# Kernel optimization log

Hardware: AMD Instinct MI355X
Metric: run time of the kernel (lower is better)

The kernel has to match this reference:

```python
import jax, jax.numpy as jnp
import numpy as np

EPS = 1e-5
HEADS = 8


def _bn(x, p):
    # p: [4, C] rows = (gamma, beta, running_mean, running_var); channel axis = 1 (eval-mode BN)
    shape = (1, p.shape[1]) + (1,) * (x.ndim - 2)
    g = p[0].reshape(shape); b = p[1].reshape(shape)
    m = p[2].reshape(shape); v = p[3].reshape(shape)
    return (x - m) * (g / jnp.sqrt(v + EPS)) + b


def _conv1x1(x, w):
    # x: [N, Cin, H, W], w: [Cout, Cin]
    return jnp.einsum('oc,nchw->nohw', w, x)


def _axial(x, kqv_w, kqv_bn, logits_bn, rel_enc, ks, height_dim):
    # x: [B, C, H, W]
    if height_dim:
        x = jnp.transpose(x, (0, 3, 1, 2))  # [B, W, C, H] -> attend over H (=ks)
    else:
        x = jnp.transpose(x, (0, 2, 1, 3))  # [B, H, C, W] -> attend over W (=ks)
    b, w, d, h = x.shape
    dh = d // HEADS
    xf = x.reshape(b * w, d, h)
    kqv = jnp.einsum('oc,ncl->nol', kqv_w, xf)          # conv1d k=1, [n, 2d, h]
    kqv = _bn(kqv, kqv_bn)
    kqv = kqv.reshape(b * w, HEADS, dh * 2, h)
    k = kqv[:, :, : dh // 2]                            # [n, H, dh/2, h]
    q = kqv[:, :, dh // 2: dh]                          # [n, H, dh/2, h]
    v = kqv[:, :, dh:]                                  # [n, H, dh,   h]
    # relative position encodings
    idx = jnp.arange(ks)[None, :] - jnp.arange(ks)[:, None] + ks - 1  # [ks, ks]
    rel = rel_enc[:, idx.reshape(-1)].reshape(dh * 2, ks, ks)
    q_enc = rel[: dh // 2]
    k_enc = rel[dh // 2: dh]
    v_enc = rel[dh:]
    qk = jnp.einsum('nhdx,nhdy->nhxy', q, k)
    qr = jnp.einsum('nhdx,dxy->nhxy', q, q_enc)
    kr = jnp.einsum('nhdx,dxy->nhyx', k, k_enc)         # einsum + transpose(2,3)
    logits = jnp.concatenate([qk, qr, kr], axis=1)       # [n, 3*H, h, h]
    logits = _bn(logits, logits_bn)
    logits = logits.reshape(b * w, 3, HEADS, h, h).sum(axis=1)
    weights = jax.nn.softmax(logits, axis=3)             # [n, H, h, h]
    attn = jnp.einsum('nhxy,nhdy->nhdx', weights, v)
    attn_enc = jnp.einsum('nhxy,dxy->nhdx', weights, v_enc)
    # cat along last dim + reshape + sum(dim=-2) in torch == elementwise sum here
    out = (attn + attn_enc).reshape(b, w, d, h)
    if height_dim:
        out = jnp.transpose(out, (0, 2, 3, 1))  # [B, C, H, W]
    else:
        out = jnp.transpose(out, (0, 2, 1, 3))  # [B, C, H, W]
    return out


def setup_inputs() -> dict:
    key = jax.random.key(0)
    ks = jax.random.split(key, 13)
    def rn(k, shape, s=0.05):
        return jax.random.normal(k, shape, jnp.float32) * s
    def rp(k, shape):
        return jax.random.uniform(k, shape, jnp.float32, minval=0.1, maxval=1.0)
    return {
        'x': jax.random.normal(ks[0], (1, 64, 256, 128), jnp.float32),
        'conv1_w': rn(ks[1], (64, 64)),
        'bn1': rp(ks[2], (4, 64)),
        'kqv_w_h': rn(ks[3], (128, 64)),
        'kqv_bn_h': rp(ks[4], (4, 128)),
        'logits_bn_h': rp(ks[5], (4, 24)),
        'rel_enc_h': rn(ks[6], (16, 511)),
        'kqv_w_w': rn(ks[7], (128, 64)),
        'kqv_bn_w': rp(ks[8], (4, 128)),
        'logits_bn_w': rp(ks[9], (4, 24)),
        'rel_enc_w': rn(ks[10], (16, 255)),
        'conv3_w': rn(ks[11], (64, 64)),
        'bn3': rp(ks[12], (4, 64)),
    }


def reference(x, conv1_w, bn1, kqv_w_h, kqv_bn_h, logits_bn_h, rel_enc_h,
              kqv_w_w, kqv_bn_w, logits_bn_w, rel_enc_w, conv3_w, bn3):
    out = jax.nn.relu(_bn(_conv1x1(x, conv1_w), bn1))
    out = _axial(out, kqv_w_h, kqv_bn_h, logits_bn_h, rel_enc_h, 256, True)
    out = _axial(out, kqv_w_w, kqv_bn_w, logits_bn_w, rel_enc_w, 128, False)
    out = jax.nn.relu(out)
    out = _bn(_conv1x1(out, conv3_w), bn3)
    return jax.nn.relu(out + x)
```

## Files before the change

### kernel.cpp

```cpp
#include <hip/hip_runtime.h>
#include <stdint.h>

#define EPSF 1e-5f
#define LOG2E 1.4426950408889634f

typedef float f32x2 __attribute__((ext_vector_type(2)));
typedef float f32x4 __attribute__((ext_vector_type(4)));

__device__ __forceinline__ float bflo(uint32_t u){ union{uint32_t u;float f;}c; c.u=u<<16; return c.f; }
__device__ __forceinline__ float bfhi(uint32_t u){ union{uint32_t u;float f;}c; c.u=u&0xffff0000u; return c.f; }
__device__ __forceinline__ float bfhiraw(uint32_t u){ union{uint32_t u;float f;}c; c.u=u; return c.f; }
__device__ __forceinline__ uint32_t f2bf(float f){ union{float f;uint32_t u;}c; c.f=f; uint32_t u=c.u; return (u + 0x7fffu + ((u>>16)&1u)) >> 16; }
__device__ __forceinline__ uint32_t pk2(float a, float b){ return f2bf(a) | (f2bf(b)<<16); }

__global__ void k_relpack(const float* __restrict__ relH, const float* __restrict__ relW,
                          uint4* __restrict__ rqkH, uint4* __restrict__ rveH,
                          uint4* __restrict__ rqkW, uint4* __restrict__ rveW) {
  int NJ = blockIdx.x ? 255 : 511;
  const float* rel = blockIdx.x ? relW : relH;
  uint4* rqk = blockIdx.x ? rqkW : rqkH;
  uint4* rve = blockIdx.x ? rveW : rveH;
  int j = threadIdx.x;
  if (j >= NJ) return;
  const float* q = rel;
  const float* k = rel + 4*NJ;
  const float* v = rel + 8*NJ;
  int jr = NJ-1-j;
  uint4 a;
  a.x = pk2(q[0*NJ+j], q[1*NJ+j]);
  a.y = pk2(q[2*NJ+j], q[3*NJ+j]);
  a.z = pk2(k[0*NJ+jr], k[1*NJ+jr]);
  a.w = pk2(k[2*NJ+jr], k[3*NJ+jr]);
  rqk[j] = a;
  uint4 b;
  b.x = pk2(v[0*NJ+j], v[1*NJ+j]);
  b.y = pk2(v[2*NJ+j], v[3*NJ+j]);
  b.z = pk2(v[4*NJ+j], v[5*NJ+j]);
  b.w = pk2(v[6*NJ+j], v[7*NJ+j]);
  rve[j] = b;
}

__global__ __launch_bounds__(256)
void k_conv1(const float* __restrict__ in, const float* __restrict__ w,
             const float* __restrict__ bn, float* __restrict__ out) {
  __shared__ float L[64*65];
  int tid = threadIdx.x;
  int p0 = blockIdx.x * 64;
  int lane = tid & 63;
  int wvs = __builtin_amdgcn_readfirstlane(tid >> 6);
  #pragma unroll
  for (int rr = 0; rr < 16; ++rr) {
    int c = wvs*16 + rr;
    L[lane*65 + c] = in[(size_t)c*32768 + p0 + lane];
  }
  __syncthreads();
  f32x2 xv2[32];
  #pragma unroll
  for (int c2 = 0; c2 < 32; ++c2) {
    xv2[c2].x = L[lane*65 + 2*c2];
    xv2[c2].y = L[lane*65 + 2*c2 + 1];
  }
  float val[16];
  #pragma unroll
  for (int r = 0; r < 16; ++r) {
    int o = wvs*16 + r;
    const f32x2* wr = (const f32x2*)(w + o*64);
    f32x2 a2 = {0.f, 0.f};
    #pragma unroll
    for (int c2 = 0; c2 < 32; ++c2) a2 = wr[c2]*xv2[c2] + a2;
    float acc = a2.x + a2.y;
    float s = bn[o] * rsqrtf(bn[192+o] + EPSF);
    val[r] = fmaxf(fmaf(acc, s, fmaf(-bn[128+o], s, bn[64+o])), 0.f);
  }
  __syncthreads();
  #pragma unroll
  for (int r = 0; r < 16; ++r) L[lane*65 + wvs*16 + r] = val[r];
  __syncthreads();
  float4* dst = (float4*)(out + (size_t)p0*64);
  #pragma unroll
  for (int k = 0; k < 4; ++k) {
    int f4 = tid + k*256;
    int f = f4*4; int p = f >> 6, o = f & 63;
    float4 v;
    v.x = L[p*65+o]; v.y = L[p*65+o+1]; v.z = L[p*65+o+2]; v.w = L[p*65+o+3];
    dst[f4] = v;
  }
}

template<int LEN, int RS, int CS>
__global__ __launch_bounds__(512)
void k_kqv(const float* __restrict__ in, const float* __restrict__ w,
           const float* __restrict__ bn, uint4* __restrict__ kvV,
           uint2* __restrict__ kvK, float* __restrict__ qb) {
  __shared__ float L[64*65];
  int tid = threadIdx.x;
  int n = blockIdx.x;
  int y0 = blockIdx.y * 64;
  #pragma unroll
  for (int rr = 0; rr < 8; ++rr) {
    int idx = tid + rr*512;
    int yy = idx >> 6, c = idx & 63;
    L[yy*65 + c] = in[((size_t)(y0+yy)*RS + (size_t)n*CS)*64 + c];
  }
  __syncthreads();
  int hd = __builtin_amdgcn_readfirstlane(tid >> 6);
  int yy = tid & 63;
  f32x2 xv2[32];
  #pragma unroll
  for (int c2 = 0; c2 < 32; ++c2) {
    xv2[c2].x = L[yy*65 + 2*c2];
    xv2[c2].y = L[yy*65 + 2*c2 + 1];
  }
  float val[16];
  #pragma unroll
  for (int r = 0; r < 16; ++r) {
    int o = hd*16 + r;
    const f32x2* wr = (const f32x2*)(w + o*64);
    f32x2 a2 = {0.f, 0.f};
    #pragma unroll
    for (int c2 = 0; c2 < 32; ++c2) a2 = wr[c2]*xv2[c2] + a2;
    float acc = a2.x + a2.y;
    float s = bn[o] * rsqrtf(bn[384+o] + EPSF);
    val[r] = fmaf(acc, s, fmaf(-bn[256+o], s, bn[128+o]));
  }
  size_t base = ((size_t)n*8 + hd)*LEN + (y0 + yy);
  kvK[base] = make_uint2(pk2(val[0],val[1]), pk2(val[2],val[3]));
  kvV[base] = make_uint4(pk2(val[8],val[9]),  pk2(val[10],val[11]),
                         pk2(val[12],val[13]), pk2(val[14],val[15]));
  float4 qq; qq.x = val[4]; qq.y = val[5]; qq.z = val[6]; qq.w = val[7];
  *(float4*)(qb + base*4) = qq;
}

template<int LEN, int G, bool RELUO, int XS, int NS>
__global__ __launch_bounds__(LEN*G/2, 2)
void k_attn2(const uint4* __restrict__ kvV, const uint2* __restrict__ kvK,
             const float* __restrict__ qb, const uint4* __restrict__ rqk,
             const uint4* __restrict__ rve, const float* __restrict__ lbn,
             float* __restrict__ out) {
  constexpr int NJ = 2*LEN-1;
  constexpr int HALF = LEN/2;
  constexpr int T = LEN*G/2;
  constexpr int YR = LEN/G;
  constexpr int CH = 4;
  constexpr size_t S1 = (size_t)LEN*64 + (size_t)NJ*48;
  constexpr size_t S2 = (size_t)(G-1)*LEN*40;
  constexpr size_t PS = S1 > S2 ? S1 : S2;
  int n  = blockIdx.x >> 3;
  int hd = blockIdx.x & 7;
  int t  = threadIdx.x;

  __shared__ __align__(16) char pool[PS];
  f32x4* sKt = (f32x4*)(pool);
  f32x4* sKr = (f32x4*)(pool + (size_t)LEN*16);
  f32x4* sVa = (f32x4*)(pool + (size_t)LEN*32);
  f32x4* sVb = (f32x4*)(pool + (size_t)LEN*48);
  f32x4* sQE = (f32x4*)(pool + (size_t)LEN*64);
  f32x4* sKE = (f32x4*)(pool + (size_t)LEN*64 + (size_t)NJ*16);
  uint4* sVE = (uint4*)(pool + (size_t)LEN*64 + (size_t)NJ*32);

  float A0L, A1L, A2L;
  {
    int c0 = hd, c1 = 8+hd, c2 = 16+hd;
    A0L = lbn[c0]*rsqrtf(lbn[72+c0]+EPSF)*LOG2E;
    A1L = lbn[c1]*rsqrtf(lbn[72+c1]+EPSF)*LOG2E;
    A2L = lbn[c2]*rsqrtf(lbn[72+c2]+EPSF)*LOG2E;
  }

  size_t kvbase = ((size_t)n*8 + hd)*LEN;
  for (int i = t; i < LEN; i += T) {
    uint2 kk = kvK[kvbase + i];
    uint4 vv = kvV[kvbase + i];
    float k0=bflo(kk.x), k1=bfhi(kk.x), k2=bflo(kk.y), k3=bfhi(kk.y);
    f32x4 kt; kt.x=k0*A0L; kt.y=k1*A0L; kt.z=k2*A0L; kt.w=k3*A0L;
    sKt[i] = kt;
    f32x4 kr; kr.x=k0; kr.y=k1; kr.z=k2; kr.w=k3;
    sKr[i] = kr;
    f32x4 va; va.x=bflo(vv.x); va.y=bfhi(vv.x); va.z=bflo(vv.y); va.w=bfhi(vv.y);
    sVa[i] = va;
    f32x4 vb; vb.x=bflo(vv.z); vb.y=bfhi(vv.z); vb.z=bflo(vv.w); vb.w=bfhi(vv.w);
    sVb[i] = vb;
  }
  for (int j = t; j < NJ; j += T) {
    uint4 a = rqk[j];
    f32x4 qe; qe.x=bflo(a.x)*A1L; qe.y=bfhi(a.x)*A1L; qe.z=bflo(a.y)*A1L; qe.w=bfhi(a.y)*A1L;
    sQE[j] = qe;
    f32x4 ke; ke.x=bflo(a.z)*A2L; ke.y=bfhi(a.z)*A2L; ke.z=bflo(a.w)*A2L; ke.w=bfhi(a.w)*A2L;
    sKE[j] = ke;
    sVE[j] = rve[j];
  }

  int g  = t / HALF;
  int tl = t % HALF;
  int y0 = g * YR;

  f32x4 qv[2];
  qv[0] = *(const f32x4*)(qb + (kvbase + tl)*4);
  qv[1] = *(const f32x4*)(qb + (kvbase + tl + HALF)*4);

  float m[2], ss[2], lr[2][CH];
  f32x2 acc2[2][4];
  #pragma unroll
  for (int i=0;i<2;++i){ m[i]=-3.0e38f; ss[i]=0.f;
    #pragma unroll
    for(int d=0;d<4;++d){ acc2[i][d].x=0.f; acc2[i][d].y=0.f; } }

  __syncthreads();

  for (int yc = 0; yc < YR; yc += CH) {
    #pragma unroll
    for (int c = 0; c < CH; ++c) {
      int y = y0 + yc + c;
      f32x4 kt = sKt[y];
      f32x4 kr = sKr[y];
      #pragma unroll
      for (int i = 0; i < 2; ++i) {
        int j = y - (tl + i*HALF) + (LEN-1);
        f32x4 qe = sQE[j];
        f32x4 ke = sKE[j];
        f32x2 t0 = kt.lo + qe.lo;
        f32x2 t1 = kt.hi + qe.hi;
        f32x2 s = qv[i].lo*t0 + qv[i].hi*t1;
        s = kr.lo*ke.lo + s;
        s = kr.hi*ke.hi + s;
        lr[i][c] = s.x + s.y;
      }
    }
    #pragma unroll
    for (int i = 0; i < 2; ++i) {
      float cm = fmaxf(fmaxf(lr[i][0], lr[i][1]), fmaxf(lr[i][2], lr[i][3]));
      float mn = fmaxf(m[i], cm);
      float sc = __builtin_amdgcn_exp2f(m[i] - mn);
      m[i] = mn; ss[i] *= sc;
      f32x2 sc2 = {sc, sc};
      #pragma unroll
      for (int d = 0; d < 4; ++d) acc2[i][d] *= sc2;
    }
    #pragma unroll
    for (int c = 0; c < CH; ++c) {
      int y = y0 + yc + c;
      f32x4 va = sVa[y], vb = sVb[y];
      #pragma unroll
      for (int i = 0; i < 2; ++i) {
        int j = y - (tl + i*HALF) + (LEN-1);
        uint4 ve = sVE[j];
        float e = __builtin_amdgcn_exp2f(lr[i][c] - m[i]);
        ss[i] += e;
        f32x2 e2 = {e, e};
        f32x2 w0; w0.x = bflo(ve.x); w0.y = bfhiraw(ve.x); w0 = va.lo + w0;
        f32x2 w1; w1.x = bflo(ve.y); w1.y = bfhiraw(ve.y); w1 = va.hi + w1;
        f32x2 w2; w2.x = bflo(ve.z); w2.y = bfhiraw(ve.z); w2 = vb.lo + w2;
        f32x2 w3; w3.x = bflo(ve.w); w3.y = bfhiraw(ve.w); w3 = vb.hi + w3;
        acc2[i][0] = e2*w0 + acc2[i][0];
        acc2[i][1] = e2*w1 + acc2[i][1];
        acc2[i][2] = e2*w2 + acc2[i][2];
        acc2[i][3] = e2*w3 + acc2[i][3];
      }
    }
  }

  __syncthreads();
  float4* M0 = (float4*)(pool);
  float4* M1 = (float4*)(pool + (size_t)(G-1)*LEN*16);
  float2* MS = (float2*)(pool + (size_t)(G-1)*LEN*32);
  if (g > 0) {
    #pragma unroll
    for (int i = 0; i < 2; ++i) {
      int slot = ((g-1)*HALF + tl)*2 + i;
      M0[slot] = make_float4(acc2[i][0].x,acc2[i][0].y,acc2[i][1].x,acc2[i][1].y);
      M1[slot] = make_float4(acc2[i][2].x,acc2[i][2].y,acc2[i][3].x,acc2[i][3].y);
      MS[slot] = make_float2(m[i], ss[i]);
    }
  }
  __syncthreads();
  if (g == 0) {
    #pragma unroll
    for (int i = 0; i < 2; ++i) {
      float M = m[i];
      float2 oms[G-1];
      #pragma unroll
      for (int gg = 1; gg < G; ++gg) {
        oms[gg-1] = MS[((gg-1)*HALF + tl)*2 + i];
        M = fmaxf(M, oms[gg-1].x);
      }
      float w0 = __builtin_amdgcn_exp2f(m[i] - M);
      float st = ss[i]*w0;
      float a[8];
      a[0]=acc2[i][0].x*w0; a[1]=acc2[i][0].y*w0; a[2]=acc2[i][1].x*w0; a[3]=acc2[i][1].y*w0;
      a[4]=acc2[i][2].x*w0; a[5]=acc2[i][2].y*w0; a[6]=acc2[i][3].x*w0; a[7]=acc2[i][3].y*w0;
      #pragma unroll
      for (int gg = 1; gg < G; ++gg) {
        int slot = ((gg-1)*HALF + tl)*2 + i;
        float wg = __builtin_amdgcn_exp2f(oms[gg-1].x - M);
        st += oms[gg-1].y*wg;
        float4 a0 = M0[slot];
        float4 a1 = M1[slot];
        a[0] = fmaf(a0.x, wg, a[0]); a[1] = fmaf(a0.y, wg, a[1]);
        a[2] = fmaf(a0.z, wg, a[2]); a[3] = fmaf(a0.w, wg, a[3]);
        a[4] = fmaf(a1.x, wg, a[4]); a[5] = fmaf(a1.y, wg, a[5]);
        a[6] = fmaf(a1.z, wg, a[6]); a[7] = fmaf(a1.w, wg, a[7]);
      }
      float inv = 1.0f / st;
      int x = tl + i*HALF;
      float* dst = out + ((size_t)x*XS + (size_t)n*NS)*64 + hd*8;
      float4 lo, hi;
      lo.x = a[0]*inv; lo.y = a[1]*inv; lo.z = a[2]*inv; lo.w = a[3]*inv;
      hi.x = a[4]*inv; hi.y = a[5]*inv; hi.z = a[6]*inv; hi.w = a[7]*inv;
      if (RELUO) {
        lo.x=fmaxf(lo.x,0.f); lo.y=fmaxf(lo.y,0.f); lo.z=fmaxf(lo.z,0.f); lo.w=fmaxf(lo.w,0.f);
        hi.x=fmaxf(hi.x,0.f); hi.y=fmaxf(hi.y,0.f); hi.z=fmaxf(hi.z,0.f); hi.w=fmaxf(hi.w,0.f);
      }
      *(float4*)dst = lo;
      *((float4*)dst + 1) = hi;
    }
  }
}

__global__ __launch_bounds__(256)
void k_conv3(const float* __restrict__ in, const float* __restrict__ w,
             const float* __restrict__ bn, const float* __restrict__ resid,
             float* __restrict__ out) {
  __shared__ float L[64*65];
  int tid = threadIdx.x;
  int p0 = blockIdx.x * 64;
  const float4* src = (const float4*)(in + (size_t)p0*64);
  #pragma unroll
  for (int k = 0; k < 4; ++k) {
    int f4 = tid + k*256;
    float4 v = src[f4];
    int f = f4*4; int p = f >> 6, o = f & 63;
    L[p*65+o] = v.x; L[p*65+o+1] = v.y; L[p*65+o+2] = v.z; L[p*65+o+3] = v.w;
  }
  __syncthreads();
  int lane = tid & 63;
  int wvs = __builtin_amdgcn_readfirstlane(tid >> 6);
  f32x2 xv2[32];
  #pragma unroll
  for (int c2 = 0; c2 < 32; ++c2) {
    xv2[c2].x = L[lane*65 + 2*c2];
    xv2[c2].y = L[lane*65 + 2*c2 + 1];
  }
  #pragma unroll
  for (int r = 0; r < 16; ++r) {
    int o = wvs*16 + r;
    const f32x2* wr = (const f32x2*)(w + o*64);
    f32x2 a2 = {0.f, 0.f};
    #pragma unroll
    for (int c2 = 0; c2 < 32; ++c2) a2 = wr[c2]*xv2[c2] + a2;
    float acc = a2.x + a2.y;
    float s = bn[o] * rsqrtf(bn[192+o] + EPSF);
    float val = fmaf(acc, s, fmaf(-bn[128+o], s, bn[64+o]));
    size_t idx = (size_t)o*32768 + p0 + lane;
    out[idx] = fmaxf(val + resid[idx], 0.f);
  }
}

extern "C" void kernel_launch(void* const* d_in, const int* in_sizes, int n_in,
                              void* d_out, int out_size, void* d_ws, size_t ws_size,
                              hipStream_t stream) {
  const float* x         = (const float*)d_in[0];
  const float* conv1_w   = (const float*)d_in[1];
  const float* bn1       = (const float*)d_in[2];
  const float* kqv_w_h   = (const float*)d_in[3];
  const float* kqv_bn_h  = (const float*)d_in[4];
  const float* lbn_h     = (const float*)d_in[5];
  const float* rel_h     = (const float*)d_in[6];
  const float* kqv_w_w   = (const float*)d_in[7];
  const float* kqv_bn_w  = (const float*)d_in[8];
  const float* lbn_w     = (const float*)d_in[9];
  const float* rel_w     = (const float*)d_in[10];
  const float* conv3_w   = (const float*)d_in[11];
  const float* bn3       = (const float*)d_in[12];
  float* outp = (float*)d_out;
  char* ws = (char*)d_ws;

  float* A    = (float*)(ws);
  uint4* kvV  = (uint4*)(ws + 8388608);
  uint2* kvK  = (uint2*)(ws + 12582912);
  float* qb   = (float*)(ws + 14680064);
  uint4* rqkH = (uint4*)(ws + 18874368);
  uint4* rveH = (uint4*)(ws + 18882560);
  uint4* rqkW = (uint4*)(ws + 18890752);
  uint4* rveW = (uint4*)(ws + 18894848);

  k_relpack<<<2, 512, 0, stream>>>(rel_h, rel_w, rqkH, rveH, rqkW, rveW);

  k_conv1<<<512, 256, 0, stream>>>(x, conv1_w, bn1, A);

  k_kqv<256,128,1><<<dim3(128,4), 512, 0, stream>>>(A, kqv_w_h, kqv_bn_h, kvV, kvK, qb);
  k_attn2<256,4,false,128,1><<<1024, 512, 0, stream>>>(kvV, kvK, qb, rqkH, rveH, lbn_h, A);

  k_kqv<128,1,128><<<dim3(256,2), 512, 0, stream>>>(A, kqv_w_w, kqv_bn_w, kvV, kvK, qb);
  k_attn2<128,4,true,1,128><<<2048, 256, 0, stream>>>(kvV, kvK, qb, rqkW, rveW, lbn_w, A);

  k_conv3<<<512, 256, 0, stream>>>(A, conv3_w, bn3, x, outp);
}
```

Measured before the change: 187.0 us.

## Register-tile four queries per thread with sliding rel-encoding window in axial attention

Each attention thread now handles four consecutive query positions instead of two. Because the relative index j = y - x shifts by one per step, the relative-encoding entries loaded from shared memory are reused across the 4x4 query/key tile through a sliding register window, cutting LDS traffic. The key-side relative term is folded algebraically into the q·k product via a ratio A2L/A0L, which drops the separate unscaled key array. The packed q/k encodings are stored in bf16 in a 4-way interleaved layout. Threads per block are halved, and register pressure rises; bf16 rounding of the scaled encodings and the ratio guard may slightly change numerics.

```diff
diff --git a/kernel.cpp b/kernel.cpp
--- a/kernel.cpp
+++ b/kernel.cpp
@@ -131,18 +131,45 @@
   *(float4*)(qb + base*4) = qq;
 }
 
+struct Acc { f32x2 a[4]; };
+
+__device__ __forceinline__ float pairA(f32x4 qv, uint4 e, f32x4 kt) {
+  f32x2 qe0; qe0.x = bflo(e.x); qe0.y = bfhiraw(e.x);
+  f32x2 qe1; qe1.x = bflo(e.y); qe1.y = bfhiraw(e.y);
+  f32x2 ke0; ke0.x = bflo(e.z); ke0.y = bfhiraw(e.z);
+  f32x2 ke1; ke1.x = bflo(e.w); ke1.y = bfhiraw(e.w);
+  f32x2 t0 = qv.lo + ke0;
+  f32x2 t1 = qv.hi + ke1;
+  f32x2 s = t0*kt.lo;
+  s = t1*kt.hi + s;
+  s = qv.lo*qe0 + s;
+  s = qv.hi*qe1 + s;
+  return s.x + s.y;
+}
+
+__device__ __forceinline__ void pairB(float ex, uint4 e, f32x4 va, f32x4 vb,
+                                      Acc& A, float& ss) {
+  ss += ex;
+  f32x2 e2; e2.x = ex; e2.y = ex;
+  f32x2 w;
+  w.x = bflo(e.x); w.y = bfhiraw(e.x); w = va.lo + w; A.a[0] = e2*w + A.a[0];
+  w.x = bflo(e.y); w.y = bfhiraw(e.y); w = va.hi + w; A.a[1] = e2*w + A.a[1];
+  w.x = bflo(e.z); w.y = bfhiraw(e.z); w = vb.lo + w; A.a[2] = e2*w + A.a[2];
+  w.x = bflo(e.w); w.y = bfhiraw(e.w); w = vb.hi + w; A.a[3] = e2*w + A.a[3];
+}
+
 template<int LEN, int G, bool RELUO, int XS, int NS>
-__global__ __launch_bounds__(LEN*G/2, 2)
-void k_attn2(const uint4* __restrict__ kvV, const uint2* __restrict__ kvK,
+__global__ __launch_bounds__(LEN/4*G, 2)
+void k_attn4(const uint4* __restrict__ kvV, const uint2* __restrict__ kvK,
              const float* __restrict__ qb, const uint4* __restrict__ rqk,
              const uint4* __restrict__ rve, const float* __restrict__ lbn,
              float* __restrict__ out) {
   constexpr int NJ = 2*LEN-1;
-  constexpr int HALF = LEN/2;
-  constexpr int T = LEN*G/2;
+  constexpr int NJ4 = (NJ+1)/4;
+  constexpr int XT = LEN/4;
+  constexpr int T = XT*G;
   constexpr int YR = LEN/G;
-  constexpr int CH = 4;
-  constexpr size_t S1 = (size_t)LEN*64 + (size_t)NJ*48;
+  constexpr size_t S1 = (size_t)LEN*48 + (size_t)NJ4*4*16*2;
   constexpr size_t S2 = (size_t)(G-1)*LEN*40;
   constexpr size_t PS = S1 > S2 ? S1 : S2;
   int n  = blockIdx.x >> 3;
@@ -151,12 +178,10 @@
 
   __shared__ __align__(16) char pool[PS];
   f32x4* sKt = (f32x4*)(pool);
-  f32x4* sKr = (f32x4*)(pool + (size_t)LEN*16);
-  f32x4* sVa = (f32x4*)(pool + (size_t)LEN*32);
-  f32x4* sVb = (f32x4*)(pool + (size_t)LEN*48);
-  f32x4* sQE = (f32x4*)(pool + (size_t)LEN*64);
-  f32x4* sKE = (f32x4*)(pool + (size_t)LEN*64 + (size_t)NJ*16);
-  uint4* sVE = (uint4*)(pool + (size_t)LEN*64 + (size_t)NJ*32);
+  f32x4* sVa = (f32x4*)(pool + (size_t)LEN*16);
+  f32x4* sVb = (f32x4*)(pool + (size_t)LEN*32);
+  uint4* tQK = (uint4*)(pool + (size_t)LEN*48);
+  uint4* tVE = (uint4*)(pool + (size_t)LEN*48 + (size_t)NJ4*64);
 
   float A0L, A1L, A2L;
   {
@@ -165,16 +190,15 @@
     A1L = lbn[c1]*rsqrtf(lbn[72+c1]+EPSF)*LOG2E;
     A2L = lbn[c2]*rsqrtf(lbn[72+c2]+EPSF)*LOG2E;
   }
+  float A0g = (fabsf(A0L) > 1e-25f) ? A0L : copysignf(1e-25f, A0L);
+  float ratio = A2L / A0g;
 
   size_t kvbase = ((size_t)n*8 + hd)*LEN;
   for (int i = t; i < LEN; i += T) {
     uint2 kk = kvK[kvbase + i];
     uint4 vv = kvV[kvbase + i];
-    float k0=bflo(kk.x), k1=bfhi(kk.x), k2=bflo(kk.y), k3=bfhi(kk.y);
-    f32x4 kt; kt.x=k0*A0L; kt.y=k1*A0L; kt.z=k2*A0L; kt.w=k3*A0L;
+    f32x4 kt; kt.x=bflo(kk.x)*A0g; kt.y=bfhi(kk.x)*A0g; kt.z=bflo(kk.y)*A0g; kt.w=bfhi(kk.y)*A0g;
     sKt[i] = kt;
-    f32x4 kr; kr.x=k0; kr.y=k1; kr.z=k2; kr.w=k3;
-    sKr[i] = kr;
     f32x4 va; va.x=bflo(vv.x); va.y=bfhi(vv.x); va.z=bflo(vv.y); va.w=bfhi(vv.y);
     sVa[i] = va;
     f32x4 vb; vb.x=bflo(vv.z); vb.y=bfhi(vv.z); vb.z=bflo(vv.w); vb.w=bfhi(vv.w);
@@ -182,80 +206,96 @@
   }
   for (int j = t; j < NJ; j += T) {
     uint4 a = rqk[j];
-    f32x4 qe; qe.x=bflo(a.x)*A1L; qe.y=bfhi(a.x)*A1L; qe.z=bflo(a.y)*A1L; qe.w=bfhi(a.y)*A1L;
-    sQE[j] = qe;
-    f32x4 ke; ke.x=bflo(a.z)*A2L; ke.y=bfhi(a.z)*A2L; ke.z=bflo(a.w)*A2L; ke.w=bfhi(a.w)*A2L;
-    sKE[j] = ke;
-    sVE[j] = rve[j];
-  }
-
-  int g  = t / HALF;
-  int tl = t % HALF;
+    uint4 sq;
+    sq.x = pk2(bflo(a.x)*A1L,   bfhi(a.x)*A1L);
+    sq.y = pk2(bflo(a.y)*A1L,   bfhi(a.y)*A1L);
+    sq.z = pk2(bflo(a.z)*ratio, bfhi(a.z)*ratio);
+    sq.w = pk2(bflo(a.w)*ratio, bfhi(a.w)*ratio);
+    int r = j & 3, mm = j >> 2;
+    tQK[r*NJ4 + mm] = sq;
+    tVE[r*NJ4 + mm] = rve[j];
+  }
+
+  int g  = t / XT;
+  int tl = t % XT;
   int y0 = g * YR;
-
-  f32x4 qv[2];
-  qv[0] = *(const f32x4*)(qb + (kvbase + tl)*4);
-  qv[1] = *(const f32x4*)(qb + (kvbase + tl + HALF)*4);
-
-  float m[2], ss[2], lr[2][CH];
-  f32x2 acc2[2][4];
-  #pragma unroll
-  for (int i=0;i<2;++i){ m[i]=-3.0e38f; ss[i]=0.f;
-    #pragma unroll
-    for(int d=0;d<4;++d){ acc2[i][d].x=0.f; acc2[i][d].y=0.f; } }
-
-  __syncthreads();
-
-  for (int yc = 0; yc < YR; yc += CH) {
-    #pragma unroll
-    for (int c = 0; c < CH; ++c) {
-      int y = y0 + yc + c;
-      f32x4 kt = sKt[y];
-      f32x4 kr = sKr[y];
-      #pragma unroll
-      for (int i = 0; i < 2; ++i) {
-        int j = y - (tl + i*HALF) + (LEN-1);
-        f32x4 qe = sQE[j];
-        f32x4 ke = sKE[j];
-        f32x2 t0 = kt.lo + qe.lo;
-        f32x2 t1 = kt.hi + qe.hi;
-        f32x2 s = qv[i].lo*t0 + qv[i].hi*t1;
-        s = kr.lo*ke.lo + s;
-        s = kr.hi*ke.hi + s;
-        lr[i][c] = s.x + s.y;
-      }
-    }
-    #pragma unroll
-    for (int i = 0; i < 2; ++i) {
+  int x0 = 4 * tl;
+
+  f32x4 q[4];
+  #pragma unroll
+  for (int i = 0; i < 4; ++i)
+    q[i] = *(const f32x4*)(qb + (kvbase + x0 + i)*4);
+
+  float m[4], ss[4];
+  Acc acc[4];
+  #pragma unroll
+  for (int i=0;i<4;++i){ m[i]=-3.0e38f; ss[i]=0.f;
+    #pragma unroll
+    for(int d=0;d<4;++d){ acc[i].a[d].x=0.f; acc[i].a[d].y=0.f; } }
+
+  __syncthreads();
+
+  int mi = ((y0 + LEN-1) >> 2) - tl;
+  uint4 wq0 = tQK[0*NJ4 + mi], wq1 = tQK[1*NJ4 + mi], wq2 = tQK[2*NJ4 + mi];
+  uint4 wv0 = tVE[0*NJ4 + mi], wv1 = tVE[1*NJ4 + mi], wv2 = tVE[2*NJ4 + mi];
+
+  for (int cc = 0; cc < YR/4; ++cc) {
+    int yb = y0 + 4*cc;
+    int ma = mi + cc;
+    int mb = ma + 1;
+    float lr[4][4];
+    uint4 e3 = tQK[3*NJ4 + ma];
+    { f32x4 kt = sKt[yb];
+      lr[0][0]=pairA(q[0],e3,kt);  lr[1][0]=pairA(q[1],wq2,kt);
+      lr[2][0]=pairA(q[2],wq1,kt); lr[3][0]=pairA(q[3],wq0,kt); }
+    uint4 e0 = tQK[0*NJ4 + mb];
+    { f32x4 kt = sKt[yb+1];
+      lr[0][1]=pairA(q[0],e0,kt);  lr[1][1]=pairA(q[1],e3,kt);
+      lr[2][1]=pairA(q[2],wq2,kt); lr[3][1]=pairA(q[3],wq1,kt); }
+    uint4 e1 = tQK[1*NJ4 + mb];
+    { f32x4 kt = sKt[yb+2];
+      lr[0][2]=pairA(q[0],e1,kt);  lr[1][2]=pairA(q[1],e0,kt);
+      lr[2][2]=pairA(q[2],e3,kt);  lr[3][2]=pairA(q[3],wq2,kt); }
+    uint4 e2v = tQK[2*NJ4 + mb];
+    { f32x4 kt = sKt[yb+3];
+      lr[0][3]=pairA(q[0],e2v,kt); lr[1][3]=pairA(q[1],e1,kt);
+      lr[2][3]=pairA(q[2],e0,kt);  lr[3][3]=pairA(q[3],e3,kt); }
+    wq0 = e0; wq1 = e1; wq2 = e2v;
+    #pragma unroll
+    for (int i = 0; i < 4; ++i) {
       float cm = fmaxf(fmaxf(lr[i][0], lr[i][1]), fmaxf(lr[i][2], lr[i][3]));
       float mn = fmaxf(m[i], cm);
       float sc = __builtin_amdgcn_exp2f(m[i] - mn);
       m[i] = mn; ss[i] *= sc;
-      f32x2 sc2 = {sc, sc};
+      f32x2 sc2; sc2.x = sc; sc2.y = sc;
       #pragma unroll
-      for (int d = 0; d < 4; ++d) acc2[i][d] *= sc2;
+      for (int d = 0; d < 4; ++d) acc[i].a[d] *= sc2;
     }
-    #pragma unroll
-    for (int c = 0; c < CH; ++c) {
-      int y = y0 + yc + c;
-      f32x4 va = sVa[y], vb = sVb[y];
-      #pragma unroll
-      for (int i = 0; i < 2; ++i) {
-        int j = y - (tl + i*HALF) + (LEN-1);
-        uint4 ve = sVE[j];
-        float e = __builtin_amdgcn_exp2f(lr[i][c] - m[i]);
-        ss[i] += e;
-        f32x2 e2 = {e, e};
-        f32x2 w0; w0.x = bflo(ve.x); w0.y = bfhiraw(ve.x); w0 = va.lo + w0;
-        f32x2 w1; w1.x = bflo(ve.y); w1.y = bfhiraw(ve.y); w1 = va.hi + w1;
-        f32x2 w2; w2.x = bflo(ve.z); w2.y = bfhiraw(ve.z); w2 = vb.lo + w2;
-        f32x2 w3; w3.x = bflo(ve.w); w3.y = bfhiraw(ve.w); w3 = vb.hi + w3;
-        acc2[i][0] = e2*w0 + acc2[i][0];
-        acc2[i][1] = e2*w1 + acc2[i][1];
-        acc2[i][2] = e2*w2 + acc2[i][2];
-        acc2[i][3] = e2*w3 + acc2[i][3];
-      }
-    }
+    uint4 f3 = tVE[3*NJ4 + ma];
+    { f32x4 va = sVa[yb], vb = sVb[yb];
+      pairB(__builtin_amdgcn_exp2f(lr[0][0]-m[0]), f3,  va, vb, acc[0], ss[0]);
+      pairB(__builtin_amdgcn_exp2f(lr[1][0]-m[1]), wv2, va, vb, acc[1], ss[1]);
+      pairB(__builtin_amdgcn_exp2f(lr[2][0]-m[2]), wv1, va, vb, acc[2], ss[2]);
+      pairB(__builtin_amdgcn_exp2f(lr[3][0]-m[3]), wv0, va, vb, acc[3], ss[3]); }
+    uint4 f0 = tVE[0*NJ4 + mb];
+    { f32x4 va = sVa[yb+1], vb = sVb[yb+1];
+      pairB(__builtin_amdgcn_exp2f(lr[0][1]-m[0]), f0,  va, vb, acc[0], ss[0]);
+      pairB(__builtin_amdgcn_exp2f(lr[1][1]-m[1]), f3,  va, vb, acc[1], ss[1]);
+      pairB(__builtin_amdgcn_exp2f(lr[2][1]-m[2]), wv2, va, vb, acc[2], ss[2]);
+      pairB(__builtin_amdgcn_exp2f(lr[3][1]-m[3]), wv1, va, vb, acc[3], ss[3]); }
+    uint4 f1 = tVE[1*NJ4 + mb];
+    { f32x4 va = sVa[yb+2], vb = sVb[yb+2];
+      pairB(__builtin_amdgcn_exp2f(lr[0][2]-m[0]), f1,  va, vb, acc[0], ss[0]);
+      pairB(__builtin_amdgcn_exp2f(lr[1][2]-m[1]), f0,  va, vb, acc[1], ss[1]);
+      pairB(__builtin_amdgcn_exp2f(lr[2][2]-m[2]), f3,  va, vb, acc[2], ss[2]);
+      pairB(__builtin_amdgcn_exp2f(lr[3][2]-m[3]), wv2, va, vb, acc[3], ss[3]); }
+    uint4 f2v = tVE[2*NJ4 + mb];
+    { f32x4 va = sVa[yb+3], vb = sVb[yb+3];
+      pairB(__builtin_amdgcn_exp2f(lr[0][3]-m[0]), f2v, va, vb, acc[0], ss[0]);
+      pairB(__builtin_amdgcn_exp2f(lr[1][3]-m[1]), f1,  va, vb, acc[1], ss[1]);
+      pairB(__builtin_amdgcn_exp2f(lr[2][3]-m[2]), f0,  va, vb, acc[2], ss[2]);
+      pairB(__builtin_amdgcn_exp2f(lr[3][3]-m[3]), f3,  va, vb, acc[3], ss[3]); }
+    wv0 = f0; wv1 = f1; wv2 = f2v;
   }
 
   __syncthreads();
@@ -264,32 +304,32 @@
   float2* MS = (float2*)(pool + (size_t)(G-1)*LEN*32);
   if (g > 0) {
     #pragma unroll
-    for (int i = 0; i < 2; ++i) {
-      int slot = ((g-1)*HALF + tl)*2 + i;
-      M0[slot] = make_float4(acc2[i][0].x,acc2[i][0].y,acc2[i][1].x,acc2[i][1].y);
-      M1[slot] = make_float4(acc2[i][2].x,acc2[i][2].y,acc2[i][3].x,acc2[i][3].y);
+    for (int i = 0; i < 4; ++i) {
+      int slot = (g-1)*LEN + x0 + i;
+      M0[slot] = make_float4(acc[i].a[0].x,acc[i].a[0].y,acc[i].a[1].x,acc[i].a[1].y);
+      M1[slot] = make_float4(acc[i].a[2].x,acc[i].a[2].y,acc[i].a[3].x,acc[i].a[3].y);
       MS[slot] = make_float2(m[i], ss[i]);
     }
   }
   __syncthreads();
   if (g == 0) {
     #pragma unroll
-    for (int i = 0; i < 2; ++i) {
+    for (int i = 0; i < 4; ++i) {
       float M = m[i];
       float2 oms[G-1];
       #pragma unroll
       for (int gg = 1; gg < G; ++gg) {
-        oms[gg-1] = MS[((gg-1)*HALF + tl)*2 + i];
+        oms[gg-1] = MS[(gg-1)*LEN + x0 + i];
         M = fmaxf(M, oms[gg-1].x);
       }
       float w0 = __builtin_amdgcn_exp2f(m[i] - M);
       float st = ss[i]*w0;
       float a[8];
-      a[0]=acc2[i][0].x*w0; a[1]=acc2[i][0].y*w0; a[2]=acc2[i][1].x*w0; a[3]=acc2[i][1].y*w0;
-      a[4]=acc2[i][2].x*w0; a[5]=acc2[i][2].y*w0; a[6]=acc2[i][3].x*w0; a[7]=acc2[i][3].y*w0;
+      a[0]=acc[i].a[0].x*w0; a[1]=acc[i].a[0].y*w0; a[2]=acc[i].a[1].x*w0; a[3]=acc[i].a[1].y*w0;
+      a[4]=acc[i].a[2].x*w0; a[5]=acc[i].a[2].y*w0; a[6]=acc[i].a[3].x*w0; a[7]=acc[i].a[3].y*w0;
       #pragma unroll
       for (int gg = 1; gg < G; ++gg) {
-        int slot = ((gg-1)*HALF + tl)*2 + i;
+        int slot = (gg-1)*LEN + x0 + i;
         float wg = __builtin_amdgcn_exp2f(oms[gg-1].x - M);
         st += oms[gg-1].y*wg;
         float4 a0 = M0[slot];
@@ -300,8 +340,7 @@
         a[6] = fmaf(a1.z, wg, a[6]); a[7] = fmaf(a1.w, wg, a[7]);
       }
       float inv = 1.0f / st;
-      int x = tl + i*HALF;
-      float* dst = out + ((size_t)x*XS + (size_t)n*NS)*64 + hd*8;
+      float* dst = out + ((size_t)(x0+i)*XS + (size_t)n*NS)*64 + hd*8;
       float4 lo, hi;
       lo.x = a[0]*inv; lo.y = a[1]*inv; lo.z = a[2]*inv; lo.w = a[3]*inv;
       hi.x = a[4]*inv; hi.y = a[5]*inv; hi.z = a[6]*inv; hi.w = a[7]*inv;
@@ -387,10 +426,10 @@
   k_conv1<<<512, 256, 0, stream>>>(x, conv1_w, bn1, A);
 
   k_kqv<256,128,1><<<dim3(128,4), 512, 0, stream>>>(A, kqv_w_h, kqv_bn_h, kvV, kvK, qb);
-  k_attn2<256,4,false,128,1><<<1024, 512, 0, stream>>>(kvV, kvK, qb, rqkH, rveH, lbn_h, A);
+  k_attn4<256,4,false,128,1><<<1024, 256, 0, stream>>>(kvV, kvK, qb, rqkH, rveH, lbn_h, A);
 
   k_kqv<128,1,128><<<dim3(256,2), 512, 0, stream>>>(A, kqv_w_w, kqv_bn_w, kvV, kvK, qb);
-  k_attn2<128,4,true,1,128><<<2048, 256, 0, stream>>>(kvV, kvK, qb, rqkW, rveW, lbn_w, A);
+  k_attn4<128,4,true,1,128><<<2048, 128, 0, stream>>>(kvV, kvK, qb, rqkW, rveW, lbn_w, A);
 
   k_conv3<<<512, 256, 0, stream>>>(A, conv3_w, bn3, x, outp);
 }
```

Result: faster. 177.7 us (-5.0%).
